# Kernel optimization log

Measured on AMD Instinct MI355X. Metric: run time of the kernel, lower is better.

Reference implementation:

```python
import jax, jax.numpy as jnp
import numpy as np

B, T, V, E, H, L = 64, 512, 100, 100, 256, 8


def _lstm_layer(xs, w_ih, w_hh, b_ih, b_hh):
    # xs: [B, T, I]; PyTorch gate order: i, f, g, o
    gx = jnp.einsum('bti,gi->btg', xs, w_ih) + b_ih  # [B, T, 4H]
    gx = jnp.swapaxes(gx, 0, 1)                      # [T, B, 4H]
    w_hh_t = w_hh.T                                  # [H, 4H]
    h0 = jnp.zeros((xs.shape[0], w_hh.shape[1]), xs.dtype)

    def step(carry, g):
        h, c = carry
        g = g + h @ w_hh_t + b_hh
        i, f, gg, o = jnp.split(g, 4, axis=-1)
        c = jax.nn.sigmoid(f) * c + jax.nn.sigmoid(i) * jnp.tanh(gg)
        h = jax.nn.sigmoid(o) * jnp.tanh(c)
        return (h, c), h

    (hT, cT), ys = jax.lax.scan(step, (h0, h0), gx)
    return jnp.swapaxes(ys, 0, 1), hT, cT


def setup_inputs() -> dict:
    key = jax.random.key(0)
    ks = jax.random.split(key, 9)
    s = 0.05  # roughly PyTorch's 1/sqrt(H) uniform scale
    return {
        'x': jax.random.randint(ks[0], (B, T), 0, V),
        'embed': jax.random.normal(ks[1], (V, E), jnp.float32) * s,
        'w_ih0': jax.random.normal(ks[2], (4 * H, E), jnp.float32) * s,
        'w_ih': jax.random.normal(ks[3], (L - 1, 4 * H, H), jnp.float32) * s,
        'w_hh': jax.random.normal(ks[4], (L, 4 * H, H), jnp.float32) * s,
        'b_ih': jax.random.normal(ks[5], (L, 4 * H), jnp.float32) * s,
        'b_hh': jax.random.normal(ks[6], (L, 4 * H), jnp.float32) * s,
        'fc_w': jax.random.normal(ks[7], (V, H), jnp.float32) * s,
        'fc_b': jax.random.normal(ks[8], (V,), jnp.float32) * s,
    }


def reference(x, embed, w_ih0, w_ih, w_hh, b_ih, b_hh, fc_w, fc_b):
    h = embed[x]  # [B, T, E]
    h_fin, c_fin = [], []
    for l in range(L):
        wih = w_ih0 if l == 0 else w_ih[l - 1]
        h, hT, cT = _lstm_layer(h, wih, w_hh[l], b_ih[l], b_hh[l])
        h_fin.append(hT)
        c_fin.append(cT)
    logits = jnp.einsum('bth,vh->btv', h, fc_w) + fc_b  # [B, T, V]
    return logits, jnp.stack(h_fin), jnp.stack(c_fin)
```

## Files before the change

kernel.cpp:

```cpp
#include <hip/hip_runtime.h>


typedef _Float16 f16;
typedef f16  f16x8 __attribute__((ext_vector_type(8)));
typedef f16  f16x4 __attribute__((ext_vector_type(4)));
typedef float f32x4 __attribute__((ext_vector_type(4)));
typedef int   i32x4 __attribute__((ext_vector_type(4)));

#define DEV __device__ __forceinline__

constexpr int TT = 512, BB = 64, VV = 100, HH = 256, LL = 8;
constexpr int RING_D = 64;

constexpr size_t XE_OFF = 0;
constexpr size_t XE_SZ  = (size_t)TT*BB*256*2;
constexpr size_t WP_OFF = XE_OFF + XE_SZ;
constexpr size_t WP_SZ  = (size_t)LL*16*64*512*2;
constexpr size_t BI_OFF = WP_OFF + WP_SZ;
constexpr size_t BI_SZ  = (size_t)LL*16*64*4;
constexpr size_t FW_OFF = BI_OFF + BI_SZ;
constexpr size_t FW_SZ  = (size_t)112*256*2;
constexpr size_t H7_OFF = FW_OFF + FW_SZ;
constexpr size_t H7_SZ  = (size_t)TT*BB*256*2;
constexpr size_t RG_OFF = H7_OFF + H7_SZ;
constexpr size_t RG_SZ  = (size_t)7*RING_D*BB*256*2;
constexpr size_t FP_OFF = RG_OFF + RG_SZ;
constexpr size_t FP_SZ  = (size_t)LL*TT*2*16;
constexpr size_t FCF_OFF = FP_OFF + FP_SZ;
constexpr size_t FCF_SZ  = (size_t)7*TT*2*16;

DEV void glc_load_issue(i32x4& d, const void* p) {
  asm volatile("global_load_dwordx4 %0, %1, off sc0 sc1" : "=v"(d) : "v"(p));
}
DEV void glc_wait0() {
  asm volatile("s_waitcnt vmcnt(0)" ::: "memory");
  __builtin_amdgcn_sched_barrier(0);
}
DEV void glc_store16(void* p, i32x4 d) {
  asm volatile("global_store_dwordx4 %0, %1, off sc0 sc1" :: "v"(p), "v"(d) : "memory");
}
DEV void flag_store(unsigned char* p) {
  int one = 1;
  asm volatile("global_store_byte %0, %1, off sc0 sc1" :: "v"(p), "v"(one) : "memory");
}
DEV bool poll16(const unsigned char* p) {
  for (int it = 0; it < (1 << 22); ++it) {
    i32x4 f;
    asm volatile("global_load_dwordx4 %0, %1, off sc0 sc1\n\ts_waitcnt vmcnt(0)"
                 : "=v"(f) : "v"(p) : "memory");
    if ((f[0] & f[1] & f[2] & f[3]) == 0x01010101) return true;
    __builtin_amdgcn_s_sleep(2);
  }
  return false;
}

DEV float sigf(float x)   { return __builtin_amdgcn_rcpf(1.f + __expf(-x)); }
DEV float tanhf2(float x) { return 1.f - 2.f * __builtin_amdgcn_rcpf(1.f + __expf(2.f * x)); }
DEV unsigned short f16bits(float v) { f16 h = (f16)v; return __builtin_bit_cast(unsigned short, h); }

__global__ void prep_zero(unsigned int* p) {
  p[blockIdx.x * 256 + threadIdx.x] = 0;
}

__global__ void prep_embed(const int* __restrict__ x, const float* __restrict__ em,
                           f16* __restrict__ xe) {
  int g = blockIdx.x * 256 + threadIdx.x;
  int chunk = g & 7, pair = g >> 3;
  int b = pair & 63, t = pair >> 6;
  int idx = x[b * 512 + t];
  const float* er = em + (size_t)idx * 100;
  f16* o = xe + (size_t)pair * 256 + chunk * 32;
  #pragma unroll
  for (int c4 = 0; c4 < 32; c4 += 4) {
    f16x4 v;
    #pragma unroll
    for (int q = 0; q < 4; ++q) {
      int c = chunk * 32 + c4 + q;
      v[q] = (c < 100) ? (f16)er[c] : (f16)0.f;
    }
    *(f16x4*)(o + c4) = v;
  }
}

__global__ void prep_w(const float* __restrict__ w_ih0, const float* __restrict__ w_ih,
                       const float* __restrict__ w_hh, f16* __restrict__ wpo) {
  int g = blockIdx.x * 256 + threadIdx.x;
  int k4 = (g & 127) * 4;
  int n  = (g >> 7) & 63;
  int ls = g >> 13;
  int l = ls >> 4, si = ls & 15;
  int r = 256 * (n & 3) + 16 * si + (n >> 2);
  f16x4 v;
  #pragma unroll
  for (int q = 0; q < 4; ++q) {
    int k = k4 + q;
    float f;
    if (k < 256) {
      if (l == 0) f = (k < 100) ? w_ih0[(size_t)r * 100 + k] : 0.f;
      else        f = w_ih[((size_t)(l - 1) * 1024 + r) * 256 + k];
    } else        f = w_hh[((size_t)l * 1024 + r) * 256 + (k - 256)];
    v[q] = (f16)f;
  }
  *(f16x4*)(wpo + (size_t)g * 4) = v;
}

__global__ void prep_bias(const float* __restrict__ b_ih, const float* __restrict__ b_hh,
                          float* __restrict__ bo) {
  int g = blockIdx.x * 256 + threadIdx.x;
  int n = g & 63, si = (g >> 6) & 15, l = g >> 10;
  int r = 256 * (n & 3) + 16 * si + (n >> 2);
  bo[g] = b_ih[l * 1024 + r] + b_hh[l * 1024 + r];
}

__global__ void prep_fcw(const float* __restrict__ fc_w, f16* __restrict__ fo) {
  int g = blockIdx.x * 256 + threadIdx.x;
  int n = g >> 6, k4 = (g & 63) * 4;
  f16x4 v;
  #pragma unroll
  for (int q = 0; q < 4; ++q)
    v[q] = (n < 100) ? (f16)fc_w[(size_t)n * 256 + k4 + q] : (f16)0.f;
  *(f16x4*)(fo + (size_t)g * 4) = v;
}

__global__ void __launch_bounds__(256, 1) lstm_pipe(
    const f16* __restrict__ xe, const f16* __restrict__ wp, const float* __restrict__ biasp,
    f16* h7, f16* rings, unsigned char* fpf, unsigned char* fcf, float* out)
{
  __shared__ float lds_part[2][32][68];
  __shared__ unsigned short lds_pub[32][16];

  const int bx  = blockIdx.x;
  const int lyr = bx & 7;
  const int sub = bx >> 3;
  const int hb  = sub & 1;
  const int sl  = sub >> 1;
  const int tid = threadIdx.x;
  const int wv  = tid >> 6;
  const int ln  = tid & 63;
  const int mt  = wv & 1;
  const int kh  = wv >> 1;

  f16x8 wf0[8], wf1[8], wf2[8], wf3[8];
  {
    const f16* wb = wp + ((size_t)(lyr * 16 + sl)) * 64 * 512;
    int n15 = ln & 15, kof = (ln >> 4) * 8;
    #pragma unroll
    for (int kt = 0; kt < 8; ++kt) {
      int k = (kh * 8 + kt) * 32 + kof;
      wf0[kt] = *(const f16x8*)(wb + (size_t)(n15)*512 + k);
      wf1[kt] = *(const f16x8*)(wb + (size_t)(16 + n15) * 512 + k);
      wf2[kt] = *(const f16x8*)(wb + (size_t)(32 + n15) * 512 + k);
      wf3[kt] = *(const f16x8*)(wb + (size_t)(48 + n15) * 512 + k);
    }
  }
  float bias8[8];
  {
    const float* bb = biasp + (size_t)(lyr * 16 + sl) * 64 + (ln & 7) * 8;
    #pragma unroll
    for (int j = 0; j < 8; ++j) bias8[j] = bb[j];
  }
  const int grow = wv * 8 + (ln >> 3);
  const int gc0  = (ln & 7) * 8;
  float c0 = 0.f, c1 = 0.f;

  const f16* xsb = (lyr == 0) ? xe : rings + (size_t)(lyr - 1) * RING_D * 16384;
  const f16* hsb = (lyr == 7) ? h7 : rings + (size_t)lyr * RING_D * 16384;
  f16*       dsb = (lyr == 7) ? h7 : rings + (size_t)lyr * RING_D * 16384;

  const int arow = 32 * hb + mt * 16 + (ln & 15);
  const int akof = (ln >> 4) * 8;

  bool dead = false;

  for (int t = 0; t < TT; ++t) {
    if (kh == 0) {
      if (lyr > 0 && !dead)
        dead = !poll16(fpf + ((size_t)((lyr - 1) * TT + t) * 2 + hb) * 16);
    } else {
      if (t > 0 && !dead)
        dead = !poll16(fpf + ((size_t)(lyr * TT + (t - 1)) * 2 + hb) * 16);
    }

    i32x4 af[8];
    if (kh == 1 && t == 0) {
      #pragma unroll
      for (int kt = 0; kt < 8; ++kt) af[kt] = i32x4{0, 0, 0, 0};
    } else {
      const f16* src;
      if (kh == 0) src = xsb + (size_t)(lyr == 0 ? t : (t & (RING_D - 1))) * 16384;
      else         src = hsb + (size_t)(lyr == 7 ? (t - 1) : ((t - 1) & (RING_D - 1))) * 16384;
      const f16* lp = src + (size_t)arow * 256 + akof;
      #pragma unroll
      for (int kt = 0; kt < 8; ++kt) glc_load_issue(af[kt], lp + kt * 32);
      glc_wait0();
    }

    f32x4 a0 = {0,0,0,0}, a1 = {0,0,0,0}, a2 = {0,0,0,0}, a3 = {0,0,0,0};
    #pragma unroll
    for (int kt = 0; kt < 8; ++kt) {
      f16x8 av = __builtin_bit_cast(f16x8, af[kt]);
      a0 = __builtin_amdgcn_mfma_f32_16x16x32_f16(av, wf0[kt], a0, 0, 0, 0);
      a1 = __builtin_amdgcn_mfma_f32_16x16x32_f16(av, wf1[kt], a1, 0, 0, 0);
      a2 = __builtin_amdgcn_mfma_f32_16x16x32_f16(av, wf2[kt], a2, 0, 0, 0);
      a3 = __builtin_amdgcn_mfma_f32_16x16x32_f16(av, wf3[kt], a3, 0, 0, 0);
    }
    {
      int pr = mt * 16 + (ln >> 4) * 4;
      int pc = ln & 15;
      #pragma unroll
      for (int j = 0; j < 4; ++j) {
        lds_part[kh][pr + j][pc]      = a0[j];
        lds_part[kh][pr + j][16 + pc] = a1[j];
        lds_part[kh][pr + j][32 + pc] = a2[j];
        lds_part[kh][pr + j][48 + pc] = a3[j];
      }
    }
    __syncthreads();
    if (lyr > 0 && tid == 0)
      flag_store(fcf + ((size_t)((lyr - 1) * TT + t) * 2 + hb) * 16 + sl);

    float hot0, hot1;
    {
      const float* p0 = &lds_part[0][grow][gc0];
      const float* p1 = &lds_part[1][grow][gc0];
      float g[8];
      #pragma unroll
      for (int j = 0; j < 8; ++j) g[j] = p0[j] + p1[j] + bias8[j];
      float i0 = sigf(g[0]), ff0 = sigf(g[1]), z0 = tanhf2(g[2]), o0 = sigf(g[3]);
      c0 = ff0 * c0 + i0 * z0;  hot0 = o0 * tanhf2(c0);
      float i1 = sigf(g[4]), ff1 = sigf(g[5]), z1 = tanhf2(g[6]), o1 = sigf(g[7]);
      c1 = ff1 * c1 + i1 * z1;  hot1 = o1 * tanhf2(c1);
      unsigned int pk = ((unsigned int)f16bits(hot1) << 16) | f16bits(hot0);
      *(unsigned int*)&lds_pub[grow][(ln & 7) * 2] = pk;
      if (t == TT - 1) {
        size_t ob = 3276800 + (size_t)lyr * 16384 + (size_t)(32 * hb + grow) * 256
                  + sl * 16 + (ln & 7) * 2;
        out[ob]     = hot0;  out[ob + 1]     = hot1;
        out[ob + 131072] = c0;  out[ob + 131072 + 1] = c1;
      }
    }
    __syncthreads();

    if (wv == 0) {
      if (lyr < 7 && t >= RING_D && !dead)
        dead = !poll16(fcf + ((size_t)(lyr * TT + (t - RING_D)) * 2 + hb) * 16);
      f16* dst = dsb + (size_t)(lyr == 7 ? t : (t & (RING_D - 1))) * 16384
               + (size_t)(32 * hb + (ln >> 1)) * 256 + sl * 16 + (ln & 1) * 8;
      i32x4 pd = ((const i32x4*)&lds_pub[0][0])[ln];
      glc_store16(dst, pd);
      asm volatile("s_waitcnt vmcnt(0)" ::: "memory");
      if (ln == 0)
        flag_store(fpf + ((size_t)(lyr * TT + t) * 2 + hb) * 16 + sl);
    }
  }
}

__global__ void __launch_bounds__(256, 1) fc_kernel(
    const f16* __restrict__ h7, const f16* __restrict__ fcw,
    const float* __restrict__ fcb, float* __restrict__ out)
{
  const int t  = blockIdx.x;
  const int wv = threadIdx.x >> 6;
  const int ln = threadIdx.x & 63;
  const f16* ab = h7 + (size_t)t * 16384 + (size_t)(wv * 16 + (ln & 15)) * 256 + (ln >> 4) * 8;
  f16x8 af[8];
  #pragma unroll
  for (int kt = 0; kt < 8; ++kt) af[kt] = *(const f16x8*)(ab + kt * 32);
  const int obrow = wv * 16 + (ln >> 4) * 4;
  #pragma unroll
  for (int nt = 0; nt < 7; ++nt) {
    const f16* bb = fcw + (size_t)(nt * 16 + (ln & 15)) * 256 + (ln >> 4) * 8;
    f32x4 acc = {0, 0, 0, 0};
    #pragma unroll
    for (int kt = 0; kt < 8; ++kt) {
      f16x8 bv = *(const f16x8*)(bb + kt * 32);
      acc = __builtin_amdgcn_mfma_f32_16x16x32_f16(af[kt], bv, acc, 0, 0, 0);
    }
    int vg = nt * 16 + (ln & 15);
    if (vg < VV) {
      float bias = fcb[vg];
      #pragma unroll
      for (int j = 0; j < 4; ++j)
        out[(size_t)(obrow + j) * 51200 + (size_t)t * 100 + vg] = acc[j] + bias;
    }
  }
}

extern "C" void kernel_launch(void* const* d_in, const int* in_sizes, int n_in,
                              void* d_out, int out_size, void* d_ws, size_t ws_size,
                              hipStream_t stream) {
  (void)in_sizes; (void)n_in; (void)out_size; (void)ws_size;
  const int*   x     = (const int*)d_in[0];
  const float* embed = (const float*)d_in[1];
  const float* w_ih0 = (const float*)d_in[2];
  const float* w_ih  = (const float*)d_in[3];
  const float* w_hh  = (const float*)d_in[4];
  const float* b_ih  = (const float*)d_in[5];
  const float* b_hh  = (const float*)d_in[6];
  const float* fc_w  = (const float*)d_in[7];
  const float* fc_b  = (const float*)d_in[8];
  char* ws = (char*)d_ws;
  float* out = (float*)d_out;

  prep_zero<<<240, 256, 0, stream>>>((unsigned int*)(ws + FP_OFF));
  prep_embed<<<1024, 256, 0, stream>>>(x, embed, (f16*)(ws + XE_OFF));
  prep_w<<<4096, 256, 0, stream>>>(w_ih0, w_ih, w_hh, (f16*)(ws + WP_OFF));
  prep_bias<<<32, 256, 0, stream>>>(b_ih, b_hh, (float*)(ws + BI_OFF));
  prep_fcw<<<28, 256, 0, stream>>>(fc_w, (f16*)(ws + FW_OFF));

  lstm_pipe<<<256, 256, 63744, stream>>>(
      (const f16*)(ws + XE_OFF), (const f16*)(ws + WP_OFF), (const float*)(ws + BI_OFF),
      (f16*)(ws + H7_OFF), (f16*)(ws + RG_OFF),
      (unsigned char*)(ws + FP_OFF), (unsigned char*)(ws + FCF_OFF), out);

  fc_kernel<<<512, 256, 0, stream>>>((const f16*)(ws + H7_OFF), (const f16*)(ws + FW_OFF),
                                     fc_b, out);
}
```

Baseline: 2.794 ms.

## Remove second block barrier with per-wave direct stores, double-buffered LDS, relaxed cache flags

Each wave now writes its h values straight to global memory and sets its own flag byte, and flags widen to 64 bytes per step and half-block. This removes the second __syncthreads and the LDS staging step, and the partial-sum LDS buffer is double-buffered by step parity. Readers poll the wider flags wave-wide without sleeping, and the load/store cache bits drop sc0. Activation input loads are split into two waits so MFMAs can start on the first half. Gate weights and biases are prescaled by log2(e) factors so the kernel can use exp2 directly. The risks are more flag traffic and memory-coherence hazards from the relaxed cache scope.

Result: slower. 4.514 ms (+61.6%).

```diff
diff --git a/kernel.cpp b/kernel.cpp
--- a/kernel.cpp
+++ b/kernel.cpp
@@ -25,37 +25,51 @@
 constexpr size_t RG_OFF = H7_OFF + H7_SZ;
 constexpr size_t RG_SZ  = (size_t)7*RING_D*BB*256*2;
 constexpr size_t FP_OFF = RG_OFF + RG_SZ;
-constexpr size_t FP_SZ  = (size_t)LL*TT*2*16;
+constexpr size_t FP_SZ  = (size_t)LL*TT*2*64;
 constexpr size_t FCF_OFF = FP_OFF + FP_SZ;
 constexpr size_t FCF_SZ  = (size_t)7*TT*2*16;
 
-DEV void glc_load_issue(i32x4& d, const void* p) {
-  asm volatile("global_load_dwordx4 %0, %1, off sc0 sc1" : "=v"(d) : "v"(p));
-}
-DEV void glc_wait0() {
+DEV void ag_load16(i32x4& d, const void* p) {
+  asm volatile("global_load_dwordx4 %0, %1, off sc1" : "=v"(d) : "v"(p));
+}
+DEV void ag_store4(void* p, unsigned int d) {
+  asm volatile("global_store_dword %0, %1, off sc1" :: "v"(p), "v"(d) : "memory");
+}
+DEV void flag_store(unsigned char* p) {
+  int one = 1;
+  asm volatile("global_store_byte %0, %1, off sc1" :: "v"(p), "v"(one) : "memory");
+}
+DEV void wait_vm0() {
   asm volatile("s_waitcnt vmcnt(0)" ::: "memory");
   __builtin_amdgcn_sched_barrier(0);
 }
-DEV void glc_store16(void* p, i32x4 d) {
-  asm volatile("global_store_dwordx4 %0, %1, off sc0 sc1" :: "v"(p), "v"(d) : "memory");
-}
-DEV void flag_store(unsigned char* p) {
-  int one = 1;
-  asm volatile("global_store_byte %0, %1, off sc0 sc1" :: "v"(p), "v"(one) : "memory");
+DEV void wait_vm4() {
+  asm volatile("s_waitcnt vmcnt(4)" ::: "memory");
+  __builtin_amdgcn_sched_barrier(0);
+}
+DEV bool poll64(const unsigned char* base, int ln) {
+  const unsigned char* p = base + (ln & 3) * 16;
+  for (int it = 0; it < (1 << 18); ++it) {
+    i32x4 f;
+    asm volatile("global_load_dwordx4 %0, %1, off sc1\n\ts_waitcnt vmcnt(0)"
+                 : "=v"(f) : "v"(p) : "memory");
+    if (__all((f[0] & f[1] & f[2] & f[3]) == 0x01010101)) return true;
+  }
+  return false;
 }
 DEV bool poll16(const unsigned char* p) {
-  for (int it = 0; it < (1 << 22); ++it) {
+  for (int it = 0; it < (1 << 18); ++it) {
     i32x4 f;
-    asm volatile("global_load_dwordx4 %0, %1, off sc0 sc1\n\ts_waitcnt vmcnt(0)"
+    asm volatile("global_load_dwordx4 %0, %1, off sc1\n\ts_waitcnt vmcnt(0)"
                  : "=v"(f) : "v"(p) : "memory");
     if ((f[0] & f[1] & f[2] & f[3]) == 0x01010101) return true;
-    __builtin_amdgcn_s_sleep(2);
   }
   return false;
 }
 
-DEV float sigf(float x)   { return __builtin_amdgcn_rcpf(1.f + __expf(-x)); }
-DEV float tanhf2(float x) { return 1.f - 2.f * __builtin_amdgcn_rcpf(1.f + __expf(2.f * x)); }
+DEV float sig2(float y)  { return __builtin_amdgcn_rcpf(1.f + __builtin_amdgcn_exp2f(-y)); }
+DEV float tanhp(float y) { return 1.f - 2.f * __builtin_amdgcn_rcpf(1.f + __builtin_amdgcn_exp2f(y)); }
+constexpr float C2LE = 2.8853900817779268f;
 DEV unsigned short f16bits(float v) { f16 h = (f16)v; return __builtin_bit_cast(unsigned short, h); }
 
 __global__ void prep_zero(unsigned int* p) {
@@ -90,6 +104,7 @@
   int ls = g >> 13;
   int l = ls >> 4, si = ls & 15;
   int r = 256 * (n & 3) + 16 * si + (n >> 2);
+  float scale = ((n & 3) == 2) ? 2.8853900817779268f : 1.4426950408889634f;
   f16x4 v;
   #pragma unroll
   for (int q = 0; q < 4; ++q) {
@@ -99,7 +114,7 @@
       if (l == 0) f = (k < 100) ? w_ih0[(size_t)r * 100 + k] : 0.f;
       else        f = w_ih[((size_t)(l - 1) * 1024 + r) * 256 + k];
     } else        f = w_hh[((size_t)l * 1024 + r) * 256 + (k - 256)];
-    v[q] = (f16)f;
+    v[q] = (f16)(f * scale);
   }
   *(f16x4*)(wpo + (size_t)g * 4) = v;
 }
@@ -109,7 +124,8 @@
   int g = blockIdx.x * 256 + threadIdx.x;
   int n = g & 63, si = (g >> 6) & 15, l = g >> 10;
   int r = 256 * (n & 3) + 16 * si + (n >> 2);
-  bo[g] = b_ih[l * 1024 + r] + b_hh[l * 1024 + r];
+  float scale = ((n & 3) == 2) ? 2.8853900817779268f : 1.4426950408889634f;
+  bo[g] = (b_ih[l * 1024 + r] + b_hh[l * 1024 + r]) * scale;
 }
 
 __global__ void prep_fcw(const float* __restrict__ fc_w, f16* __restrict__ fo) {
@@ -126,8 +142,7 @@
     const f16* __restrict__ xe, const f16* __restrict__ wp, const float* __restrict__ biasp,
     f16* h7, f16* rings, unsigned char* fpf, unsigned char* fcf, float* out)
 {
-  __shared__ float lds_part[2][32][68];
-  __shared__ unsigned short lds_pub[32][16];
+  __shared__ float lds_part[2][2][32][68];
 
   const int bx  = blockIdx.x;
   const int lyr = bx & 7;
@@ -169,20 +184,24 @@
 
   const int arow = 32 * hb + mt * 16 + (ln & 15);
   const int akof = (ln >> 4) * 8;
+  const int pubc = sl * 16 + (ln & 7) * 2;
 
   bool dead = false;
 
   for (int t = 0; t < TT; ++t) {
     if (kh == 0) {
       if (lyr > 0 && !dead)
-        dead = !poll16(fpf + ((size_t)((lyr - 1) * TT + t) * 2 + hb) * 16);
+        dead = !poll64(fpf + ((size_t)((lyr - 1) * TT + t) * 2 + hb) * 64, ln);
+      if (wv == 1 && lyr < 7 && t >= RING_D && !dead)
+        dead = !poll16(fcf + ((size_t)(lyr * TT + (t - RING_D)) * 2 + hb) * 16);
     } else {
       if (t > 0 && !dead)
-        dead = !poll16(fpf + ((size_t)(lyr * TT + (t - 1)) * 2 + hb) * 16);
-    }
-
+        dead = !poll64(fpf + ((size_t)(lyr * TT + (t - 1)) * 2 + hb) * 64, ln);
+    }
+
+    const bool zeroA = (kh == 1 && t == 0);
     i32x4 af[8];
-    if (kh == 1 && t == 0) {
+    if (zeroA) {
       #pragma unroll
       for (int kt = 0; kt < 8; ++kt) af[kt] = i32x4{0, 0, 0, 0};
     } else {
@@ -191,66 +210,68 @@
       else         src = hsb + (size_t)(lyr == 7 ? (t - 1) : ((t - 1) & (RING_D - 1))) * 16384;
       const f16* lp = src + (size_t)arow * 256 + akof;
       #pragma unroll
-      for (int kt = 0; kt < 8; ++kt) glc_load_issue(af[kt], lp + kt * 32);
-      glc_wait0();
+      for (int kt = 0; kt < 8; ++kt) ag_load16(af[kt], lp + kt * 32);
     }
 
     f32x4 a0 = {0,0,0,0}, a1 = {0,0,0,0}, a2 = {0,0,0,0}, a3 = {0,0,0,0};
-    #pragma unroll
-    for (int kt = 0; kt < 8; ++kt) {
+    if (!zeroA) wait_vm4();
+    #pragma unroll
+    for (int kt = 0; kt < 4; ++kt) {
       f16x8 av = __builtin_bit_cast(f16x8, af[kt]);
       a0 = __builtin_amdgcn_mfma_f32_16x16x32_f16(av, wf0[kt], a0, 0, 0, 0);
       a1 = __builtin_amdgcn_mfma_f32_16x16x32_f16(av, wf1[kt], a1, 0, 0, 0);
       a2 = __builtin_amdgcn_mfma_f32_16x16x32_f16(av, wf2[kt], a2, 0, 0, 0);
       a3 = __builtin_amdgcn_mfma_f32_16x16x32_f16(av, wf3[kt], a3, 0, 0, 0);
     }
+    if (!zeroA) wait_vm0();
+    #pragma unroll
+    for (int kt = 4; kt < 8; ++kt) {
+      f16x8 av = __builtin_bit_cast(f16x8, af[kt]);
+      a0 = __builtin_amdgcn_mfma_f32_16x16x32_f16(av, wf0[kt], a0, 0, 0, 0);
+      a1 = __builtin_amdgcn_mfma_f32_16x16x32_f16(av, wf1[kt], a1, 0, 0, 0);
+      a2 = __builtin_amdgcn_mfma_f32_16x16x32_f16(av, wf2[kt], a2, 0, 0, 0);
+      a3 = __builtin_amdgcn_mfma_f32_16x16x32_f16(av, wf3[kt], a3, 0, 0, 0);
+    }
     {
+      int par = t & 1;
       int pr = mt * 16 + (ln >> 4) * 4;
       int pc = ln & 15;
       #pragma unroll
       for (int j = 0; j < 4; ++j) {
-        lds_part[kh][pr + j][pc]      = a0[j];
-        lds_part[kh][pr + j][16 + pc] = a1[j];
-        lds_part[kh][pr + j][32 + pc] = a2[j];
-        lds_part[kh][pr + j][48 + pc] = a3[j];
+        lds_part[par][kh][pr + j][pc]      = a0[j];
+        lds_part[par][kh][pr + j][16 + pc] = a1[j];
+        lds_part[par][kh][pr + j][32 + pc] = a2[j];
+        lds_part[par][kh][pr + j][48 + pc] = a3[j];
       }
     }
     __syncthreads();
     if (lyr > 0 && tid == 0)
       flag_store(fcf + ((size_t)((lyr - 1) * TT + t) * 2 + hb) * 16 + sl);
 
-    float hot0, hot1;
     {
-      const float* p0 = &lds_part[0][grow][gc0];
-      const float* p1 = &lds_part[1][grow][gc0];
+      int par = t & 1;
+      const float* p0 = &lds_part[par][0][grow][gc0];
+      const float* p1 = &lds_part[par][1][grow][gc0];
       float g[8];
       #pragma unroll
       for (int j = 0; j < 8; ++j) g[j] = p0[j] + p1[j] + bias8[j];
-      float i0 = sigf(g[0]), ff0 = sigf(g[1]), z0 = tanhf2(g[2]), o0 = sigf(g[3]);
-      c0 = ff0 * c0 + i0 * z0;  hot0 = o0 * tanhf2(c0);
-      float i1 = sigf(g[4]), ff1 = sigf(g[5]), z1 = tanhf2(g[6]), o1 = sigf(g[7]);
-      c1 = ff1 * c1 + i1 * z1;  hot1 = o1 * tanhf2(c1);
+      float i0 = sig2(g[0]), ff0 = sig2(g[1]), z0 = tanhp(g[2]), o0 = sig2(g[3]);
+      c0 = ff0 * c0 + i0 * z0;  float hot0 = o0 * tanhp(c0 * C2LE);
+      float i1 = sig2(g[4]), ff1 = sig2(g[5]), z1 = tanhp(g[6]), o1 = sig2(g[7]);
+      c1 = ff1 * c1 + i1 * z1;  float hot1 = o1 * tanhp(c1 * C2LE);
+
       unsigned int pk = ((unsigned int)f16bits(hot1) << 16) | f16bits(hot0);
-      *(unsigned int*)&lds_pub[grow][(ln & 7) * 2] = pk;
+      f16* dst = dsb + (size_t)(lyr == 7 ? t : (t & (RING_D - 1))) * 16384
+               + (size_t)(32 * hb + grow) * 256 + pubc;
+      ag_store4(dst, pk);
       if (t == TT - 1) {
-        size_t ob = 3276800 + (size_t)lyr * 16384 + (size_t)(32 * hb + grow) * 256
-                  + sl * 16 + (ln & 7) * 2;
-        out[ob]     = hot0;  out[ob + 1]     = hot1;
+        size_t ob = 3276800 + (size_t)lyr * 16384 + (size_t)(32 * hb + grow) * 256 + pubc;
+        out[ob] = hot0;  out[ob + 1] = hot1;
         out[ob + 131072] = c0;  out[ob + 131072 + 1] = c1;
       }
-    }
-    __syncthreads();
-
-    if (wv == 0) {
-      if (lyr < 7 && t >= RING_D && !dead)
-        dead = !poll16(fcf + ((size_t)(lyr * TT + (t - RING_D)) * 2 + hb) * 16);
-      f16* dst = dsb + (size_t)(lyr == 7 ? t : (t & (RING_D - 1))) * 16384
-               + (size_t)(32 * hb + (ln >> 1)) * 256 + sl * 16 + (ln & 1) * 8;
-      i32x4 pd = ((const i32x4*)&lds_pub[0][0])[ln];
-      glc_store16(dst, pd);
-      asm volatile("s_waitcnt vmcnt(0)" ::: "memory");
+      wait_vm0();
       if (ln == 0)
-        flag_store(fpf + ((size_t)(lyr * TT + t) * 2 + hb) * 16 + sl);
+        flag_store(fpf + ((size_t)(lyr * TT + t) * 2 + hb) * 64 + sl * 4 + wv);
     }
   }
 }
@@ -302,13 +323,13 @@
   char* ws = (char*)d_ws;
   float* out = (float*)d_out;
 
-  prep_zero<<<240, 256, 0, stream>>>((unsigned int*)(ws + FP_OFF));
+  prep_zero<<<624, 256, 0, stream>>>((unsigned int*)(ws + FP_OFF));
   prep_embed<<<1024, 256, 0, stream>>>(x, embed, (f16*)(ws + XE_OFF));
   prep_w<<<4096, 256, 0, stream>>>(w_ih0, w_ih, w_hh, (f16*)(ws + WP_OFF));
   prep_bias<<<32, 256, 0, stream>>>(b_ih, b_hh, (float*)(ws + BI_OFF));
   prep_fcw<<<28, 256, 0, stream>>>(fc_w, (f16*)(ws + FW_OFF));
 
-  lstm_pipe<<<256, 256, 63744, stream>>>(
+  lstm_pipe<<<256, 256, 12544, stream>>>(
       (const f16*)(ws + XE_OFF), (const f16*)(ws + WP_OFF), (const float*)(ws + BI_OFF),
       (f16*)(ws + H7_OFF), (f16*)(ws + RG_OFF),
       (unsigned char*)(ws + FP_OFF), (unsigned char*)(ws + FCF_OFF), out);
```

## Restructure LSTM wavefront pipeline to 128 blocks with per-wave flags and no LDS reduction

Applied to the files above, without the earlier changes.

Reorganizes the layer-pipelined LSTM kernel so each block of 512 threads owns a full 64-unit slice across all 64 batch rows, with every wave computing complete gate pre-activations over the full K (input plus hidden) in registers. This removes the LDS partial-sum exchange and both __syncthreads per step. Waves publish h directly with short stores and set their own flag bytes. Polling is split across lanes (input, hidden, and ring back-pressure at once) using sc1-only loads. Weights and biases are prescaled by log2e so the activations use exp2 directly, and the ring depth is halved. The changes cut per-step latency on the serial recurrence, at the cost of more scattered 2-byte stores and a halved ring that leaves less slack between layers.

Result: slower. 7.042 ms (+152.1%).

```diff
diff --git a/kernel.cpp b/kernel.cpp
--- a/kernel.cpp
+++ b/kernel.cpp
@@ -10,7 +10,7 @@
 #define DEV __device__ __forceinline__
 
 constexpr int TT = 512, BB = 64, VV = 100, HH = 256, LL = 8;
-constexpr int RING_D = 64;
+constexpr int RING_D = 32;
 
 constexpr size_t XE_OFF = 0;
 constexpr size_t XE_SZ  = (size_t)TT*BB*256*2;
@@ -23,43 +23,42 @@
 constexpr size_t H7_OFF = FW_OFF + FW_SZ;
 constexpr size_t H7_SZ  = (size_t)TT*BB*256*2;
 constexpr size_t RG_OFF = H7_OFF + H7_SZ;
-constexpr size_t RG_SZ  = (size_t)7*RING_D*BB*256*2;
-constexpr size_t FP_OFF = RG_OFF + RG_SZ;
-constexpr size_t FP_SZ  = (size_t)LL*TT*2*16;
-constexpr size_t FCF_OFF = FP_OFF + FP_SZ;
-constexpr size_t FCF_SZ  = (size_t)7*TT*2*16;
-
-DEV void glc_load_issue(i32x4& d, const void* p) {
-  asm volatile("global_load_dwordx4 %0, %1, off sc0 sc1" : "=v"(d) : "v"(p));
-}
-DEV void glc_wait0() {
-  asm volatile("s_waitcnt vmcnt(0)" ::: "memory");
-  __builtin_amdgcn_sched_barrier(0);
-}
-DEV void glc_store16(void* p, i32x4 d) {
-  asm volatile("global_store_dwordx4 %0, %1, off sc0 sc1" :: "v"(p), "v"(d) : "memory");
-}
-DEV void flag_store(unsigned char* p) {
-  int one = 1;
-  asm volatile("global_store_byte %0, %1, off sc0 sc1" :: "v"(p), "v"(one) : "memory");
-}
-DEV bool poll16(const unsigned char* p) {
-  for (int it = 0; it < (1 << 22); ++it) {
+constexpr size_t RG_SZ  = (size_t)LL*RING_D*BB*256*2;
+constexpr size_t FPF_OFF = RG_OFF + RG_SZ;
+constexpr size_t FPF_SZ  = (size_t)LL*TT*128;
+constexpr size_t FCF_OFF = FPF_OFF + FPF_SZ;
+constexpr size_t FCF_SZ  = (size_t)7*TT*128;
+constexpr size_t ONES_OFF = FCF_OFF + FCF_SZ;
+constexpr int ZERO_DW = (int)((FPF_SZ + FCF_SZ) / 4);
+
+DEV void ld16_pl (i32x4& d, const void* p){ asm volatile("global_load_dwordx4 %0, %1, off"     : "=v"(d) : "v"(p)); }
+DEV void ld16_sc1(i32x4& d, const void* p){ asm volatile("global_load_dwordx4 %0, %1, off sc1" : "=v"(d) : "v"(p)); }
+DEV void st2_sc1(void* p, unsigned v){ asm volatile("global_store_short %0, %1, off sc1" :: "v"(p), "v"(v) : "memory"); }
+DEV void st2_pl (void* p, unsigned v){ asm volatile("global_store_short %0, %1, off"     :: "v"(p), "v"(v) : "memory"); }
+DEV void stb_sc1(void* p){ unsigned o = 1; asm volatile("global_store_byte %0, %1, off sc1" :: "v"(p), "v"(o) : "memory"); }
+DEV void wait_vm0(){ asm volatile("s_waitcnt vmcnt(0)" ::: "memory"); __builtin_amdgcn_sched_barrier(0); }
+DEV void wait_vm8(){ asm volatile("s_waitcnt vmcnt(8)" ::: "memory"); __builtin_amdgcn_sched_barrier(0); }
+
+DEV bool pollc(const unsigned char* pa) {
+  for (int it = 0; it < (1 << 19); ++it) {
     i32x4 f;
-    asm volatile("global_load_dwordx4 %0, %1, off sc0 sc1\n\ts_waitcnt vmcnt(0)"
-                 : "=v"(f) : "v"(p) : "memory");
-    if ((f[0] & f[1] & f[2] & f[3]) == 0x01010101) return true;
-    __builtin_amdgcn_s_sleep(2);
+    asm volatile("global_load_dwordx4 %0, %1, off sc1\n\ts_waitcnt vmcnt(0)"
+                 : "=v"(f) : "v"(pa) : "memory");
+    if (__all((f[0] & f[1] & f[2] & f[3]) == 0x01010101)) return true;
+    if (it > 128) __builtin_amdgcn_s_sleep(1);
   }
   return false;
 }
 
-DEV float sigf(float x)   { return __builtin_amdgcn_rcpf(1.f + __expf(-x)); }
-DEV float tanhf2(float x) { return 1.f - 2.f * __builtin_amdgcn_rcpf(1.f + __expf(2.f * x)); }
-DEV unsigned short f16bits(float v) { f16 h = (f16)v; return __builtin_bit_cast(unsigned short, h); }
-
-__global__ void prep_zero(unsigned int* p) {
+DEV float sig2(float y)  { return __builtin_amdgcn_rcpf(1.f + __builtin_amdgcn_exp2f(-y)); }
+DEV float tanhp(float y) { return 1.f - 2.f * __builtin_amdgcn_rcpf(1.f + __builtin_amdgcn_exp2f(y)); }
+constexpr float LOG2E = 1.4426950408889634f;
+constexpr float C2LE  = 2.8853900817779268f;
+DEV unsigned f16bits(float v) { f16 h = (f16)v; return (unsigned)__builtin_bit_cast(unsigned short, h); }
+
+__global__ void prep_zero(unsigned int* p, unsigned int* ones) {
   p[blockIdx.x * 256 + threadIdx.x] = 0;
+  if (blockIdx.x == 0 && threadIdx.x < 4) ones[threadIdx.x] = 0x01010101u;
 }
 
 __global__ void prep_embed(const int* __restrict__ x, const float* __restrict__ em,
@@ -88,8 +87,11 @@
   int k4 = (g & 127) * 4;
   int n  = (g >> 7) & 63;
   int ls = g >> 13;
-  int l = ls >> 4, si = ls & 15;
-  int r = 256 * (n & 3) + 16 * si + (n >> 2);
+  int l = ls >> 4, s = ls & 15;
+  int gate = n & 3;
+  int u = s * 16 + ((n >> 4) << 2) + ((n >> 2) & 3);
+  int r = 256 * gate + u;
+  float scale = (gate == 2) ? C2LE : LOG2E;
   f16x4 v;
   #pragma unroll
   for (int q = 0; q < 4; ++q) {
@@ -99,7 +101,7 @@
       if (l == 0) f = (k < 100) ? w_ih0[(size_t)r * 100 + k] : 0.f;
       else        f = w_ih[((size_t)(l - 1) * 1024 + r) * 256 + k];
     } else        f = w_hh[((size_t)l * 1024 + r) * 256 + (k - 256)];
-    v[q] = (f16)f;
+    v[q] = (f16)(f * scale);
   }
   *(f16x4*)(wpo + (size_t)g * 4) = v;
 }
@@ -107,9 +109,12 @@
 __global__ void prep_bias(const float* __restrict__ b_ih, const float* __restrict__ b_hh,
                           float* __restrict__ bo) {
   int g = blockIdx.x * 256 + threadIdx.x;
-  int n = g & 63, si = (g >> 6) & 15, l = g >> 10;
-  int r = 256 * (n & 3) + 16 * si + (n >> 2);
-  bo[g] = b_ih[l * 1024 + r] + b_hh[l * 1024 + r];
+  int n = g & 63, s = (g >> 6) & 15, l = g >> 10;
+  int gate = n & 3;
+  int u = s * 16 + ((n >> 4) << 2) + ((n >> 2) & 3);
+  int r = 256 * gate + u;
+  float scale = (gate == 2) ? C2LE : LOG2E;
+  bo[g] = (b_ih[l * 1024 + r] + b_hh[l * 1024 + r]) * scale;
 }
 
 __global__ void prep_fcw(const float* __restrict__ fc_w, f16* __restrict__ fo) {
@@ -122,136 +127,125 @@
   *(f16x4*)(fo + (size_t)g * 4) = v;
 }
 
-__global__ void __launch_bounds__(256, 1) lstm_pipe(
+__global__ void __launch_bounds__(512, 2) lstm_pipe(
     const f16* __restrict__ xe, const f16* __restrict__ wp, const float* __restrict__ biasp,
-    f16* h7, f16* rings, unsigned char* fpf, unsigned char* fcf, float* out)
+    f16* h7, f16* rings, unsigned char* fpf, unsigned char* fcf,
+    const unsigned char* ones, float* out)
 {
-  __shared__ float lds_part[2][32][68];
-  __shared__ unsigned short lds_pub[32][16];
+  static __shared__ char pad_lds[40960];
+  (void)((volatile char*)pad_lds)[threadIdx.x];
 
   const int bx  = blockIdx.x;
   const int lyr = bx & 7;
-  const int sub = bx >> 3;
-  const int hb  = sub & 1;
-  const int sl  = sub >> 1;
+  const int sl  = bx >> 3;
   const int tid = threadIdx.x;
   const int wv  = tid >> 6;
   const int ln  = tid & 63;
-  const int mt  = wv & 1;
-  const int kh  = wv >> 1;
-
-  f16x8 wf0[8], wf1[8], wf2[8], wf3[8];
+  const int mA  = wv >> 2;
+  const int nB  = wv & 3;
+
+  f16x8 wfa[2][16];
   {
-    const f16* wb = wp + ((size_t)(lyr * 16 + sl)) * 64 * 512;
-    int n15 = ln & 15, kof = (ln >> 4) * 8;
+    const f16* wb = wp + (size_t)(lyr * 16 + sl) * 64 * 512;
+    #pragma unroll
+    for (int tt = 0; tt < 2; ++tt)
+      #pragma unroll
+      for (int kt = 0; kt < 16; ++kt)
+        wfa[tt][kt] = *(const f16x8*)(wb + (size_t)((2 * mA + tt) * 16 + (ln & 15)) * 512
+                                      + kt * 32 + (ln >> 4) * 8);
+  }
+  f32x4 bias_v[2];
+  #pragma unroll
+  for (int tt = 0; tt < 2; ++tt)
+    bias_v[tt] = *(const f32x4*)(biasp + (size_t)(lyr * 16 + sl) * 64
+                                 + (2 * mA + tt) * 16 + (ln >> 4) * 4);
+
+  float cst0 = 0.f, cst1 = 0.f;
+  const int bcol = nB * 16 + (ln & 15);
+  const int kof  = (ln >> 4) * 8;
+  const f16* xring = rings + (size_t)(lyr - 1) * RING_D * 16384;
+  const f16* hring = rings + (size_t)lyr * RING_D * 16384;
+  bool dead = false;
+
+  for (int t = 0; t < TT; ++t) {
+    if (!dead) {
+      const int role = ln >> 3, chunk = (ln & 7) * 16;
+      const bool nx = (lyr > 0), nh = (t > 0), nb = (lyr < 7) && (t >= RING_D);
+      const unsigned char* px = fpf + (((size_t)(lyr - 1) * TT + t) << 7) + chunk;
+      const unsigned char* ph = fpf + (((size_t)lyr * TT + (t - 1)) << 7) + chunk;
+      const unsigned char* pb = fcf + (((size_t)lyr * TT + (t - RING_D)) << 7) + chunk;
+      const unsigned char* pa;
+      if (role == 1)      pa = nh ? ph : ones;
+      else if (role == 2) pa = nb ? pb : ones;
+      else                pa = nx ? px : (nh ? ph : ones);
+      dead = !pollc(pa);
+    }
+
+    const bool hasH = (t > 0);
+    i32x4 bfx[8], bfh[8];
+    {
+      const f16* xb = ((lyr == 0) ? xe + (size_t)t * 16384
+                                  : xring + (size_t)(t & (RING_D - 1)) * 16384)
+                      + (size_t)bcol * 256 + kof;
+      if (lyr == 0) {
+        #pragma unroll
+        for (int kt = 0; kt < 8; ++kt) ld16_pl(bfx[kt], xb + kt * 32);
+      } else {
+        #pragma unroll
+        for (int kt = 0; kt < 8; ++kt) ld16_sc1(bfx[kt], xb + kt * 32);
+      }
+      if (hasH) {
+        const f16* hb = hring + (size_t)((t - 1) & (RING_D - 1)) * 16384
+                      + (size_t)bcol * 256 + kof;
+        #pragma unroll
+        for (int kt = 0; kt < 8; ++kt) ld16_sc1(bfh[kt], hb + kt * 32);
+      }
+    }
+
+    f32x4 acc0 = {0,0,0,0}, acc1 = {0,0,0,0};
+    if (hasH) wait_vm8(); else wait_vm0();
     #pragma unroll
     for (int kt = 0; kt < 8; ++kt) {
-      int k = (kh * 8 + kt) * 32 + kof;
-      wf0[kt] = *(const f16x8*)(wb + (size_t)(n15)*512 + k);
-      wf1[kt] = *(const f16x8*)(wb + (size_t)(16 + n15) * 512 + k);
-      wf2[kt] = *(const f16x8*)(wb + (size_t)(32 + n15) * 512 + k);
-      wf3[kt] = *(const f16x8*)(wb + (size_t)(48 + n15) * 512 + k);
-    }
-  }
-  float bias8[8];
-  {
-    const float* bb = biasp + (size_t)(lyr * 16 + sl) * 64 + (ln & 7) * 8;
-    #pragma unroll
-    for (int j = 0; j < 8; ++j) bias8[j] = bb[j];
-  }
-  const int grow = wv * 8 + (ln >> 3);
-  const int gc0  = (ln & 7) * 8;
-  float c0 = 0.f, c1 = 0.f;
-
-  const f16* xsb = (lyr == 0) ? xe : rings + (size_t)(lyr - 1) * RING_D * 16384;
-  const f16* hsb = (lyr == 7) ? h7 : rings + (size_t)lyr * RING_D * 16384;
-  f16*       dsb = (lyr == 7) ? h7 : rings + (size_t)lyr * RING_D * 16384;
-
-  const int arow = 32 * hb + mt * 16 + (ln & 15);
-  const int akof = (ln >> 4) * 8;
-
-  bool dead = false;
-
-  for (int t = 0; t < TT; ++t) {
-    if (kh == 0) {
-      if (lyr > 0 && !dead)
-        dead = !poll16(fpf + ((size_t)((lyr - 1) * TT + t) * 2 + hb) * 16);
-    } else {
-      if (t > 0 && !dead)
-        dead = !poll16(fpf + ((size_t)(lyr * TT + (t - 1)) * 2 + hb) * 16);
-    }
-
-    i32x4 af[8];
-    if (kh == 1 && t == 0) {
+      f16x8 av = __builtin_bit_cast(f16x8, bfx[kt]);
+      acc0 = __builtin_amdgcn_mfma_f32_16x16x32_f16(wfa[0][kt], av, acc0, 0, 0, 0);
+      acc1 = __builtin_amdgcn_mfma_f32_16x16x32_f16(wfa[1][kt], av, acc1, 0, 0, 0);
+    }
+    if (hasH) {
+      wait_vm0();
+      if (lyr > 0 && ln == 0)
+        stb_sc1(fcf + (((size_t)(lyr - 1) * TT + t) << 7) + sl * 8 + wv);
       #pragma unroll
-      for (int kt = 0; kt < 8; ++kt) af[kt] = i32x4{0, 0, 0, 0};
-    } else {
-      const f16* src;
-      if (kh == 0) src = xsb + (size_t)(lyr == 0 ? t : (t & (RING_D - 1))) * 16384;
-      else         src = hsb + (size_t)(lyr == 7 ? (t - 1) : ((t - 1) & (RING_D - 1))) * 16384;
-      const f16* lp = src + (size_t)arow * 256 + akof;
-      #pragma unroll
-      for (int kt = 0; kt < 8; ++kt) glc_load_issue(af[kt], lp + kt * 32);
-      glc_wait0();
-    }
-
-    f32x4 a0 = {0,0,0,0}, a1 = {0,0,0,0}, a2 = {0,0,0,0}, a3 = {0,0,0,0};
-    #pragma unroll
-    for (int kt = 0; kt < 8; ++kt) {
-      f16x8 av = __builtin_bit_cast(f16x8, af[kt]);
-      a0 = __builtin_amdgcn_mfma_f32_16x16x32_f16(av, wf0[kt], a0, 0, 0, 0);
-      a1 = __builtin_amdgcn_mfma_f32_16x16x32_f16(av, wf1[kt], a1, 0, 0, 0);
-      a2 = __builtin_amdgcn_mfma_f32_16x16x32_f16(av, wf2[kt], a2, 0, 0, 0);
-      a3 = __builtin_amdgcn_mfma_f32_16x16x32_f16(av, wf3[kt], a3, 0, 0, 0);
-    }
-    {
-      int pr = mt * 16 + (ln >> 4) * 4;
-      int pc = ln & 15;
-      #pragma unroll
-      for (int j = 0; j < 4; ++j) {
-        lds_part[kh][pr + j][pc]      = a0[j];
-        lds_part[kh][pr + j][16 + pc] = a1[j];
-        lds_part[kh][pr + j][32 + pc] = a2[j];
-        lds_part[kh][pr + j][48 + pc] = a3[j];
+      for (int kt = 0; kt < 8; ++kt) {
+        f16x8 av = __builtin_bit_cast(f16x8, bfh[kt]);
+        acc0 = __builtin_amdgcn_mfma_f32_16x16x32_f16(wfa[0][8 + kt], av, acc0, 0, 0, 0);
+        acc1 = __builtin_amdgcn_mfma_f32_16x16x32_f16(wfa[1][8 + kt], av, acc1, 0, 0, 0);
       }
-    }
-    __syncthreads();
-    if (lyr > 0 && tid == 0)
-      flag_store(fcf + ((size_t)((lyr - 1) * TT + t) * 2 + hb) * 16 + sl);
-
-    float hot0, hot1;
-    {
-      const float* p0 = &lds_part[0][grow][gc0];
-      const float* p1 = &lds_part[1][grow][gc0];
-      float g[8];
-      #pragma unroll
-      for (int j = 0; j < 8; ++j) g[j] = p0[j] + p1[j] + bias8[j];
-      float i0 = sigf(g[0]), ff0 = sigf(g[1]), z0 = tanhf2(g[2]), o0 = sigf(g[3]);
-      c0 = ff0 * c0 + i0 * z0;  hot0 = o0 * tanhf2(c0);
-      float i1 = sigf(g[4]), ff1 = sigf(g[5]), z1 = tanhf2(g[6]), o1 = sigf(g[7]);
-      c1 = ff1 * c1 + i1 * z1;  hot1 = o1 * tanhf2(c1);
-      unsigned int pk = ((unsigned int)f16bits(hot1) << 16) | f16bits(hot0);
-      *(unsigned int*)&lds_pub[grow][(ln & 7) * 2] = pk;
+    } else if (lyr > 0 && ln == 0) {
+      stb_sc1(fcf + (((size_t)(lyr - 1) * TT + t) << 7) + sl * 8 + wv);
+    }
+
+    f16* rdst = rings + ((size_t)lyr * RING_D + (t & (RING_D - 1))) * 16384
+              + (size_t)bcol * 256;
+    #pragma unroll
+    for (int tt = 0; tt < 2; ++tt) {
+      f32x4 g4 = (tt == 0 ? acc0 : acc1);
+      g4 += bias_v[tt];
+      float i_ = sig2(g4[0]), f_ = sig2(g4[1]), z_ = tanhp(g4[2]), o_ = sig2(g4[3]);
+      float& c_ = (tt == 0 ? cst0 : cst1);
+      c_ = f_ * c_ + i_ * z_;
+      float h_ = o_ * tanhp(c_ * C2LE);
+      const int u = sl * 16 + (2 * mA + tt) * 4 + (ln >> 4);
+      unsigned hb16 = f16bits(h_);
+      st2_sc1(rdst + u, hb16);
+      if (lyr == 7) st2_pl(h7 + (size_t)t * 16384 + (size_t)bcol * 256 + u, hb16);
       if (t == TT - 1) {
-        size_t ob = 3276800 + (size_t)lyr * 16384 + (size_t)(32 * hb + grow) * 256
-                  + sl * 16 + (ln & 7) * 2;
-        out[ob]     = hot0;  out[ob + 1]     = hot1;
-        out[ob + 131072] = c0;  out[ob + 131072 + 1] = c1;
+        size_t ob = 3276800 + (size_t)lyr * 16384 + (size_t)bcol * 256 + u;
+        out[ob] = h_;  out[ob + 131072] = c_;
       }
     }
-    __syncthreads();
-
-    if (wv == 0) {
-      if (lyr < 7 && t >= RING_D && !dead)
-        dead = !poll16(fcf + ((size_t)(lyr * TT + (t - RING_D)) * 2 + hb) * 16);
-      f16* dst = dsb + (size_t)(lyr == 7 ? t : (t & (RING_D - 1))) * 16384
-               + (size_t)(32 * hb + (ln >> 1)) * 256 + sl * 16 + (ln & 1) * 8;
-      i32x4 pd = ((const i32x4*)&lds_pub[0][0])[ln];
-      glc_store16(dst, pd);
-      asm volatile("s_waitcnt vmcnt(0)" ::: "memory");
-      if (ln == 0)
-        flag_store(fpf + ((size_t)(lyr * TT + t) * 2 + hb) * 16 + sl);
-    }
+    wait_vm0();
+    if (ln == 0)
+      stb_sc1(fpf + (((size_t)lyr * TT + t) << 7) + sl * 8 + wv);
   }
 }
 
@@ -302,16 +296,18 @@
   char* ws = (char*)d_ws;
   float* out = (float*)d_out;
 
-  prep_zero<<<240, 256, 0, stream>>>((unsigned int*)(ws + FP_OFF));
+  prep_zero<<<960, 256, 0, stream>>>((unsigned int*)(ws + FPF_OFF),
+                                     (unsigned int*)(ws + ONES_OFF));
   prep_embed<<<1024, 256, 0, stream>>>(x, embed, (f16*)(ws + XE_OFF));
   prep_w<<<4096, 256, 0, stream>>>(w_ih0, w_ih, w_hh, (f16*)(ws + WP_OFF));
   prep_bias<<<32, 256, 0, stream>>>(b_ih, b_hh, (float*)(ws + BI_OFF));
   prep_fcw<<<28, 256, 0, stream>>>(fc_w, (f16*)(ws + FW_OFF));
 
-  lstm_pipe<<<256, 256, 63744, stream>>>(
+  lstm_pipe<<<128, 512, 41216, stream>>>(
       (const f16*)(ws + XE_OFF), (const f16*)(ws + WP_OFF), (const float*)(ws + BI_OFF),
       (f16*)(ws + H7_OFF), (f16*)(ws + RG_OFF),
-      (unsigned char*)(ws + FP_OFF), (unsigned char*)(ws + FCF_OFF), out);
+      (unsigned char*)(ws + FPF_OFF), (unsigned char*)(ws + FCF_OFF),
+      (const unsigned char*)(ws + ONES_OFF), out);
 
   fc_kernel<<<512, 256, 0, stream>>>((const f16*)(ws + H7_OFF), (const f16*)(ws + FW_OFF),
                                      fc_b, out);
```
